# Optimization experiments

Hardware: AMD Instinct MI355X
Metric: run time of the kernel (lower is better)

Reference implementation:

```python
import jax, jax.numpy as jnp
import numpy as np

HEADS = 4
DIM_HEAD = 32
SCALE = DIM_HEAD ** -0.5


def setup_inputs() -> dict:
    key = jax.random.key(0)
    k1, k2, k3 = jax.random.split(key, 3)
    dim, hidden = 256, HEADS * DIM_HEAD
    x = jax.random.normal(k1, (4, dim, 64, 64), dtype=jnp.float32)
    w_qkv = jax.random.normal(k2, (hidden * 3, dim), dtype=jnp.float32) * (dim ** -0.5)
    w_out = jax.random.normal(k3, (dim, hidden), dtype=jnp.float32) * (hidden ** -0.5)
    b_out = jnp.zeros((dim,), dtype=jnp.float32)
    return {"x": x, "w_qkv": w_qkv, "w_out": w_out, "b_out": b_out}


def reference(x, w_qkv, w_out, b_out):
    b, c, h, w = x.shape
    # 1x1 conv (no bias) == channel matmul
    qkv = jnp.einsum('bchw,oc->bohw', x, w_qkv)           # [b, 3*hidden, h, w]
    q, k, v = jnp.split(qkv, 3, axis=1)
    def to_heads(t):
        # [b, heads*d, h, w] -> [b, heads, h*w, d]
        return t.reshape(b, HEADS, DIM_HEAD, h * w).transpose(0, 1, 3, 2)
    q, k, v = to_heads(q) * SCALE, to_heads(k), to_heads(v)
    sim = jnp.einsum('bhid,bhjd->bhij', q, k)             # [b, heads, hw, hw]
    attn = jax.nn.softmax(sim, axis=-1)
    out = jnp.einsum('bhij,bhjd->bhid', attn, v)          # [b, heads, hw, d]
    out = out.transpose(0, 1, 3, 2).reshape(b, HEADS * DIM_HEAD, h, w)
    # output 1x1 conv with bias
    return jnp.einsum('bchw,oc->bohw', out, w_out) + b_out[None, :, None, None]
```

## Files before the change

kernel.cpp:

```cpp
#include <hip/hip_runtime.h>
#include <hip/hip_fp16.h>

#define HEADS 4
#define DH    32
#define HW    4096
#define CIN   256
#define HID   128
#define KSPLIT 2
#define KHALF (HW / KSPLIT)
#define NIT   (KHALF / 64)

using half8    = __attribute__((ext_vector_type(8))) _Float16;
using half4    = __attribute__((ext_vector_type(4))) _Float16;
using half2v   = __attribute__((ext_vector_type(2))) _Float16;
using floatx4  = __attribute__((ext_vector_type(4))) float;
using floatx16 = __attribute__((ext_vector_type(16))) float;
using uint4v   = __attribute__((ext_vector_type(4))) unsigned;

#define SHIFT2 4.328085122666891f
#define WQSCALE 0.25508275947f

static __device__ __forceinline__ unsigned pkr(float a, float b) {
  return __builtin_bit_cast(unsigned, __builtin_amdgcn_cvt_pkrtz(a, b));
}

__global__ __launch_bounds__(256) void qkv_fused(
    const float* __restrict__ w, const float* __restrict__ x,
    _Float16* __restrict__ Qw, _Float16* __restrict__ Kw,
    _Float16* __restrict__ Vtw)
{
  __shared__ float t[64][65];
  __shared__ _Float16 Bs[64][72];
  const int mg = blockIdx.x, nt = blockIdx.y;
  const int b = nt >> 6, p0 = (nt & 63) * 64;
  const int tid = threadIdx.x;
  const int wv = tid >> 6, lane = tid & 63, lm = lane & 15, quad = lane >> 4;

  const float* xb = x + (size_t)b * CIN * HW + p0;

  floatx4 acc[3][4] = {{{0,0,0,0},{0,0,0,0},{0,0,0,0},{0,0,0,0}},
                       {{0,0,0,0},{0,0,0,0},{0,0,0,0},{0,0,0,0}},
                       {{0,0,0,0},{0,0,0,0},{0,0,0,0},{0,0,0,0}}};

  for (int kq = 0; kq < 4; ++kq) {
    #pragma unroll
    for (int i = 0; i < 4; ++i) {
      int ci = tid + i * 256;
      int cc = ci >> 4, p4 = (ci & 15) * 4;
      *(float4*)&t[cc][p4] =
          *(const float4*)(xb + (size_t)(kq * 64 + cc) * HW + p4);
    }
    __syncthreads();
    #pragma unroll
    for (int i = 0; i < 2; ++i) {
      int idx = tid + i * 256;
      int p = idx >> 3, c0 = (idx & 7) * 8;
      half8 v;
      #pragma unroll
      for (int k = 0; k < 8; ++k) v[k] = (_Float16)t[c0 + k][p];
      *(half8*)&Bs[p][c0] = v;
    }
    __syncthreads();

    half8 bfr[2][4];
    #pragma unroll
    for (int ks = 0; ks < 2; ++ks)
      #pragma unroll
      for (int ns = 0; ns < 4; ++ns)
        bfr[ks][ns] = *(const half8*)&Bs[ns * 16 + lm][ks * 32 + quad * 8];

    #pragma unroll
    for (int im = 0; im < 3; ++im) {
      const int mt = mg * 3 + im;
      const float wscale = (mt < 2) ? WQSCALE : 1.0f;
      const float* Ag = w + (size_t)(mt * 64 + wv * 16 + lm) * CIN + kq * 64;
      #pragma unroll
      for (int ks = 0; ks < 2; ++ks) {
        const float* srcA = Ag + ks * 32 + quad * 8;
        float4 u0 = *(const float4*)(srcA);
        float4 u1 = *(const float4*)(srcA + 4);
        half8 a = {(_Float16)(u0.x * wscale), (_Float16)(u0.y * wscale),
                   (_Float16)(u0.z * wscale), (_Float16)(u0.w * wscale),
                   (_Float16)(u1.x * wscale), (_Float16)(u1.y * wscale),
                   (_Float16)(u1.z * wscale), (_Float16)(u1.w * wscale)};
        #pragma unroll
        for (int ns = 0; ns < 4; ++ns)
          acc[im][ns] = __builtin_amdgcn_mfma_f32_16x16x32_f16(a, bfr[ks][ns], acc[im][ns], 0, 0, 0);
      }
    }
  }

  #pragma unroll
  for (int im = 0; im < 3; ++im) {
    const int mt = mg * 3 + im;
    const int sec = mt >> 1;
    const int o_base = (mt & 1) * 64 + wv * 16 + quad * 4;
    const int hh = o_base >> 5, dd = o_base & 31;
    const int bh = b * HEADS + hh;
    if (sec < 2) {
      _Float16* dst = (sec == 0) ? Qw : Kw;
      #pragma unroll
      for (int ns = 0; ns < 4; ++ns) {
        int p = p0 + ns * 16 + lm;
        half4 v = {(_Float16)acc[im][ns][0], (_Float16)acc[im][ns][1],
                   (_Float16)acc[im][ns][2], (_Float16)acc[im][ns][3]};
        *(half4*)(dst + ((size_t)bh * HW + p) * DH + dd) = v;
      }
    } else {
      #pragma unroll
      for (int ns = 0; ns < 4; ++ns) {
        int p = p0 + ns * 16 + lm;
        #pragma unroll
        for (int r = 0; r < 4; ++r)
          Vtw[((size_t)bh * DH + dd + r) * HW + p] = (_Float16)acc[im][ns][r];
      }
    }
  }
}

__global__ __launch_bounds__(256) void attn(
    const _Float16* __restrict__ Qw, const _Float16* __restrict__ Kw,
    const _Float16* __restrict__ Vtw, float* __restrict__ Op,
    float* __restrict__ lp)
{
  __shared__ _Float16 ks[2][64][32];
  __shared__ _Float16 vt[2][32][64];

  const int bh = blockIdx.y, qt = blockIdx.x, z = blockIdx.z;
  const int tid = threadIdx.x;
  const int wv = tid >> 6, lane = tid & 63;
  const int l31 = lane & 31, hi = lane >> 5;

  const _Float16* qbase =
      Qw + ((size_t)bh * HW + qt * 128 + wv * 32 + l31) * DH + hi * 8;
  const half8 qb0 = *(const half8*)qbase;
  const half8 qb1 = *(const half8*)(qbase + 16);

  const floatx16 shift16 = {-SHIFT2,-SHIFT2,-SHIFT2,-SHIFT2,
                            -SHIFT2,-SHIFT2,-SHIFT2,-SHIFT2,
                            -SHIFT2,-SHIFT2,-SHIFT2,-SHIFT2,
                            -SHIFT2,-SHIFT2,-SHIFT2,-SHIFT2};
  floatx16 oT = {0,0,0,0,0,0,0,0,0,0,0,0,0,0,0,0};
  float lsum = 0.0f;

  const _Float16* kbase = Kw  + (size_t)bh * HW * DH + (size_t)z * KHALF * DH;
  const _Float16* vbase = Vtw + (size_t)bh * DH * HW + (size_t)z * KHALF;
  const int kr = tid >> 2, kls = tid & 3;
  const int vr = tid >> 3, vls = tid & 7;
  const int kps = (kls ^ (((kr >> 1) ^ (kr >> 3)) & 3)) * 8;
  const int vps = (vls ^ ((vr ^ (vr >> 3)) & 7)) * 8;
  const int kc = kls * 8, vc = vls * 8;

  const int krk = ((l31 >> 1) ^ (l31 >> 3)) & 3;
  const int vrk = (l31 ^ (l31 >> 3)) & 7;

  half8 kA = *(const half8*)(kbase + (size_t)kr * DH + kc);
  half8 vA = *(const half8*)(vbase + (size_t)vr * HW + vc);
  *(half8*)&ks[0][kr][kps] = kA;
  *(half8*)&vt[0][vr][vps] = vA;
  kA = *(const half8*)(kbase + ((size_t)64 + kr) * DH + kc);
  vA = *(const half8*)(vbase + (size_t)vr * HW + 64 + vc);
  __syncthreads();

  for (int it = 0; it < NIT; ++it) {
    const int ph = it & 1, nx = ph ^ 1;

    half8 ka[2][2];
    half8 va[4];
    #pragma unroll
    for (int t = 0; t < 2; ++t)
      #pragma unroll
      for (int d = 0; d < 2; ++d)
        ka[t][d] = *(const half8*)&ks[ph][t * 32 + l31][((d * 2 + hi) ^ krk) * 8];
    #pragma unroll
    for (int k4 = 0; k4 < 4; ++k4)
      va[k4] = *(const half8*)&vt[ph][l31][((k4 * 2 + hi) ^ vrk) * 8];

    *(half8*)&ks[nx][kr][kps] = kA;
    *(half8*)&vt[nx][vr][vps] = vA;
    size_t koff = (size_t)(it + 2) * 64;
    if (koff > KHALF - 64) koff = KHALF - 64;
    kA = *(const half8*)(kbase + (koff + kr) * DH + kc);
    vA = *(const half8*)(vbase + (size_t)vr * HW + koff + vc);

    #pragma unroll
    for (int t = 0; t < 2; ++t) {
      floatx16 sT = __builtin_amdgcn_mfma_f32_32x32x16_f16(ka[t][0], qb0, shift16, 0, 0, 0);
      sT = __builtin_amdgcn_mfma_f32_32x32x16_f16(ka[t][1], qb1, sT, 0, 0, 0);
      float e[16];
      #pragma unroll
      for (int r = 0; r < 16; ++r) e[r] = __builtin_amdgcn_exp2f(sT[r]);
      lsum += (((e[0]+e[1])+(e[2]+e[3]))+((e[4]+e[5])+(e[6]+e[7])))
            + (((e[8]+e[9])+(e[10]+e[11]))+((e[12]+e[13])+(e[14]+e[15])));
      unsigned w0 = pkr(e[0],  e[1]),  w1 = pkr(e[2],  e[3]);
      unsigned w2 = pkr(e[4],  e[5]),  w3 = pkr(e[6],  e[7]);
      unsigned w4 = pkr(e[8],  e[9]),  w5 = pkr(e[10], e[11]);
      unsigned w6 = pkr(e[12], e[13]), w7 = pkr(e[14], e[15]);
      asm("v_permlane32_swap_b32 %0, %1" : "+v"(w0), "+v"(w2));
      asm("v_permlane32_swap_b32 %0, %1" : "+v"(w1), "+v"(w3));
      asm("v_permlane32_swap_b32 %0, %1" : "+v"(w4), "+v"(w6));
      asm("v_permlane32_swap_b32 %0, %1" : "+v"(w5), "+v"(w7));
      uint4v lo4 = {w0, w1, w2, w3}, hi4 = {w4, w5, w6, w7};
      half8 pbLo = __builtin_bit_cast(half8, lo4);
      half8 pbHi = __builtin_bit_cast(half8, hi4);
      oT = __builtin_amdgcn_mfma_f32_32x32x16_f16(va[2*t],     pbLo, oT, 0, 0, 0);
      oT = __builtin_amdgcn_mfma_f32_32x32x16_f16(va[2*t + 1], pbHi, oT, 0, 0, 0);
    }
    __syncthreads();
  }

  lsum += __shfl_xor(lsum, 32, 64);
  const int b = bh >> 2, hh = bh & 3;
  const int row = qt * 128 + wv * 32 + l31;
  float* obase = Op + ((size_t)z * 4 * HW + (size_t)b * HW + row) * HID + hh * DH;
  #pragma unroll
  for (int r0 = 0; r0 < 4; ++r0) {
    float4 v = {oT[4*r0], oT[4*r0+1], oT[4*r0+2], oT[4*r0+3]};
    *(float4*)(obase + 8 * r0 + 4 * hi) = v;
  }
  if (lane < 32)
    lp[(size_t)z * HEADS * 4 * HW + (size_t)bh * HW + row] = lsum;
}

__global__ __launch_bounds__(256) void out_gemm(
    const float* __restrict__ wo, const float* __restrict__ Op,
    const float* __restrict__ lp, const float* __restrict__ bo,
    float* __restrict__ out)
{
  __shared__ _Float16 Bs[64][136];
  __shared__ float inv_l[64][4];
  const int mg = blockIdx.x, nt = blockIdx.y;
  const int b = nt >> 6, p0 = (nt & 63) * 64;
  const int tid = threadIdx.x;
  const int wv = tid >> 6, lane = tid & 63, lm = lane & 15, quad = lane >> 4;

  {
    const int p = tid >> 2, hh = tid & 3;
    const size_t qi = (size_t)(b * HEADS + hh) * HW + p0 + p;
    inv_l[p][hh] = 1.0f / (lp[qi] + lp[(size_t)HEADS * 4 * HW + qi]);
  }
  __syncthreads();

  const float* Bp0 = Op + ((size_t)b * HW + p0) * HID;
  const float* Bp1 = Bp0 + (size_t)4 * HW * HID;

  #pragma unroll
  for (int i = 0; i < 4; ++i) {
    int ci = tid + i * 256;
    int r = ci >> 4, c8 = (ci & 15) * 8;
    const float* s0 = Bp0 + (size_t)r * HID + c8;
    const float* s1 = Bp1 + (size_t)r * HID + c8;
    float4 o0 = *(const float4*)(s0);
    float4 o1 = *(const float4*)(s0 + 4);
    float4 o2 = *(const float4*)(s1);
    float4 o3 = *(const float4*)(s1 + 4);
    const float sc = inv_l[r][c8 >> 5];
    half8 hb = {(_Float16)((o0.x + o2.x) * sc), (_Float16)((o0.y + o2.y) * sc),
                (_Float16)((o0.z + o2.z) * sc), (_Float16)((o0.w + o2.w) * sc),
                (_Float16)((o1.x + o3.x) * sc), (_Float16)((o1.y + o3.y) * sc),
                (_Float16)((o1.z + o3.z) * sc), (_Float16)((o1.w + o3.w) * sc)};
    *(half8*)&Bs[r][c8] = hb;
  }
  __syncthreads();

  half8 bfr[4][4];
  #pragma unroll
  for (int ks = 0; ks < 4; ++ks)
    #pragma unroll
    for (int ns = 0; ns < 4; ++ns)
      bfr[ks][ns] = *(const half8*)&Bs[ns * 16 + lm][ks * 32 + quad * 8];

  #pragma unroll
  for (int im = 0; im < 2; ++im) {
    const int mt = mg * 2 + im;
    const float* Ag = wo + (size_t)(mt * 64 + wv * 16 + lm) * HID;

    floatx4 acc[4] = {{0,0,0,0},{0,0,0,0},{0,0,0,0},{0,0,0,0}};
    #pragma unroll
    for (int ks = 0; ks < 4; ++ks) {
      const float* srcA = Ag + ks * 32 + quad * 8;
      float4 u0 = *(const float4*)(srcA);
      float4 u1 = *(const float4*)(srcA + 4);
      half8 a = {(_Float16)u0.x, (_Float16)u0.y, (_Float16)u0.z, (_Float16)u0.w,
                 (_Float16)u1.x, (_Float16)u1.y, (_Float16)u1.z, (_Float16)u1.w};
      #pragma unroll
      for (int ns = 0; ns < 4; ++ns)
        acc[ns] = __builtin_amdgcn_mfma_f32_16x16x32_f16(a, bfr[ks][ns], acc[ns], 0, 0, 0);
    }

    const int o_loc = wv * 16 + quad * 4;
    #pragma unroll
    for (int r = 0; r < 4; ++r) {
      const int o = mt * 64 + o_loc + r;
      const float bias = bo[o];
      float* dst = out + ((size_t)(b * CIN + o)) * HW + p0 + lm;
      #pragma unroll
      for (int ns = 0; ns < 4; ++ns)
        dst[ns * 16] = acc[ns][r] + bias;
    }
  }
}

extern "C" void kernel_launch(void* const* d_in, const int* in_sizes, int n_in,
                              void* d_out, int out_size, void* d_ws, size_t ws_size,
                              hipStream_t stream)
{
  const float* x     = (const float*)d_in[0];
  const float* w_qkv = (const float*)d_in[1];
  const float* w_out = (const float*)d_in[2];
  const float* b_out = (const float*)d_in[3];
  float* out = (float*)d_out;

  char* ws = (char*)d_ws;
  _Float16* Qw  = (_Float16*)(ws);
  _Float16* Kw  = (_Float16*)(ws + (4u  << 20));
  _Float16* Vtw = (_Float16*)(ws + (8u  << 20));
  float*    Op  = (float*)   (ws + (12u << 20));
  float*    lp  = (float*)   (ws + (28u << 20));

  dim3 blk(256);
  qkv_fused<<<dim3(2, 256), blk, 0, stream>>>(w_qkv, x, Qw, Kw, Vtw);
  attn<<<dim3(32, 16, KSPLIT), blk, 0, stream>>>(Qw, Kw, Vtw, Op, lp);
  out_gemm<<<dim3(2, 256), blk, 0, stream>>>(w_out, Op, lp, b_out, out);
}
```

Measured before the change: 153.3 us.

## Load QKV B-fragments directly from global memory and halve the pixel tile

The QKV projection kernel no longer stages x through shared memory with a transpose. Each lane instead gathers its half8 B-fragment with strided scalar global loads, which removes both __syncthreads and the LDS traffic. The pixel tile shrinks from 64 to 32, so the grid doubles to 512 blocks in y for more parallelism. In exchange, the loads become uncoalesced 2-byte-stride reads across channels, and each x element is loaded by all 4 waves redundantly.

```diff
diff --git a/kernel.cpp b/kernel.cpp
--- a/kernel.cpp
+++ b/kernel.cpp
@@ -29,45 +29,31 @@
     _Float16* __restrict__ Qw, _Float16* __restrict__ Kw,
     _Float16* __restrict__ Vtw)
 {
-  __shared__ float t[64][65];
-  __shared__ _Float16 Bs[64][72];
   const int mg = blockIdx.x, nt = blockIdx.y;
-  const int b = nt >> 6, p0 = (nt & 63) * 64;
+  const int b = nt >> 7, p0 = (nt & 127) * 32;
   const int tid = threadIdx.x;
   const int wv = tid >> 6, lane = tid & 63, lm = lane & 15, quad = lane >> 4;
 
   const float* xb = x + (size_t)b * CIN * HW + p0;
 
-  floatx4 acc[3][4] = {{{0,0,0,0},{0,0,0,0},{0,0,0,0},{0,0,0,0}},
-                       {{0,0,0,0},{0,0,0,0},{0,0,0,0},{0,0,0,0}},
-                       {{0,0,0,0},{0,0,0,0},{0,0,0,0},{0,0,0,0}}};
+  floatx4 acc[3][2] = {{{0,0,0,0},{0,0,0,0}},
+                       {{0,0,0,0},{0,0,0,0}},
+                       {{0,0,0,0},{0,0,0,0}}};
 
   for (int kq = 0; kq < 4; ++kq) {
-    #pragma unroll
-    for (int i = 0; i < 4; ++i) {
-      int ci = tid + i * 256;
-      int cc = ci >> 4, p4 = (ci & 15) * 4;
-      *(float4*)&t[cc][p4] =
-          *(const float4*)(xb + (size_t)(kq * 64 + cc) * HW + p4);
-    }
-    __syncthreads();
-    #pragma unroll
-    for (int i = 0; i < 2; ++i) {
-      int idx = tid + i * 256;
-      int p = idx >> 3, c0 = (idx & 7) * 8;
-      half8 v;
-      #pragma unroll
-      for (int k = 0; k < 8; ++k) v[k] = (_Float16)t[c0 + k][p];
-      *(half8*)&Bs[p][c0] = v;
-    }
-    __syncthreads();
-
-    half8 bfr[2][4];
+    half8 bfr[2][2];
     #pragma unroll
     for (int ks = 0; ks < 2; ++ks)
       #pragma unroll
-      for (int ns = 0; ns < 4; ++ns)
-        bfr[ks][ns] = *(const half8*)&Bs[ns * 16 + lm][ks * 32 + quad * 8];
+      for (int ns = 0; ns < 2; ++ns) {
+        const float* src =
+            xb + (size_t)(kq * 64 + ks * 32 + quad * 8) * HW + ns * 16 + lm;
+        half8 bf;
+        #pragma unroll
+        for (int j = 0; j < 8; ++j)
+          bf[j] = (_Float16)src[(size_t)j * HW];
+        bfr[ks][ns] = bf;
+      }
 
     #pragma unroll
     for (int im = 0; im < 3; ++im) {
@@ -84,7 +70,7 @@
                    (_Float16)(u1.x * wscale), (_Float16)(u1.y * wscale),
                    (_Float16)(u1.z * wscale), (_Float16)(u1.w * wscale)};
         #pragma unroll
-        for (int ns = 0; ns < 4; ++ns)
+        for (int ns = 0; ns < 2; ++ns)
           acc[im][ns] = __builtin_amdgcn_mfma_f32_16x16x32_f16(a, bfr[ks][ns], acc[im][ns], 0, 0, 0);
       }
     }
@@ -100,7 +86,7 @@
     if (sec < 2) {
       _Float16* dst = (sec == 0) ? Qw : Kw;
       #pragma unroll
-      for (int ns = 0; ns < 4; ++ns) {
+      for (int ns = 0; ns < 2; ++ns) {
         int p = p0 + ns * 16 + lm;
         half4 v = {(_Float16)acc[im][ns][0], (_Float16)acc[im][ns][1],
                    (_Float16)acc[im][ns][2], (_Float16)acc[im][ns][3]};
@@ -108,7 +94,7 @@
       }
     } else {
       #pragma unroll
-      for (int ns = 0; ns < 4; ++ns) {
+      for (int ns = 0; ns < 2; ++ns) {
         int p = p0 + ns * 16 + lm;
         #pragma unroll
         for (int r = 0; r < 4; ++r)
@@ -319,7 +305,7 @@
   float*    lp  = (float*)   (ws + (28u << 20));
 
   dim3 blk(256);
-  qkv_fused<<<dim3(2, 256), blk, 0, stream>>>(w_qkv, x, Qw, Kw, Vtw);
+  qkv_fused<<<dim3(2, 512), blk, 0, stream>>>(w_qkv, x, Qw, Kw, Vtw);
   attn<<<dim3(32, 16, KSPLIT), blk, 0, stream>>>(Qw, Kw, Vtw, Op, lp);
   out_gemm<<<dim3(2, 256), blk, 0, stream>>>(w_out, Op, lp, b_out, out);
 }
```

After: 163.7 us. 1.07x slower.
